# Kernel tuning notes

Measured on AMD Instinct MI355X. Metric: run time of the kernel, lower is better.

Reference implementation:

```python
import jax, jax.numpy as jnp
import numpy as np

D_MODEL = 1024
H = 16
D_K = D_MODEL // H


def setup_inputs() -> dict:
    key = jax.random.key(0)
    ks = jax.random.split(key, 12)
    B, S = 4, 2048
    s = 1.0 / np.sqrt(D_MODEL)
    return {
        "Q": jax.random.normal(ks[0], (B, S, D_MODEL), jnp.float32),
        "K": jax.random.normal(ks[1], (B, S, D_MODEL), jnp.float32),
        "V": jax.random.normal(ks[2], (B, S, D_MODEL), jnp.float32),
        "attn_mask": jnp.ones((B, S), jnp.int32),
        "Wq": jax.random.normal(ks[3], (D_MODEL, D_MODEL), jnp.float32) * s,
        "bq": jax.random.normal(ks[4], (D_MODEL,), jnp.float32) * s,
        "Wk": jax.random.normal(ks[5], (D_MODEL, D_MODEL), jnp.float32) * s,
        "bk": jax.random.normal(ks[6], (D_MODEL,), jnp.float32) * s,
        "Wv": jax.random.normal(ks[7], (D_MODEL, D_MODEL), jnp.float32) * s,
        "bv": jax.random.normal(ks[8], (D_MODEL,), jnp.float32) * s,
        "Wo": jax.random.normal(ks[9], (D_MODEL, D_MODEL), jnp.float32) * s,
        "bo": jax.random.normal(ks[10], (D_MODEL,), jnp.float32) * s,
    }


def _split_heads(x):
    B, S, _ = x.shape
    return x.reshape(B, S, H, D_K).transpose(0, 2, 1, 3)  # (B,H,S,Dk)


def reference(Q, K, V, attn_mask, Wq, bq, Wk, bk, Wv, bv, Wo, bo):
    # Linear projections (torch Linear: x @ W.T + b)
    q = _split_heads(Q @ Wq.T + bq)
    k = _split_heads(K @ Wk.T + bk)
    v = _split_heads(V @ Wv.T + bv)
    scale = 1.0 / jnp.sqrt(jnp.asarray(D_K, q.dtype))
    scores = jnp.einsum("bhqd,bhkd->bhqk", q, k) * scale  # (B,H,S,S)
    # 2-D mask (B,S) broadcast over heads and query positions; 0 -> -inf
    mask = attn_mask[:, None, None, :]
    scores = jnp.where(mask == 0, -jnp.inf, scores)
    attn = jax.nn.softmax(scores, axis=-1)
    # dropout_proba = 0.0 -> identity
    x = jnp.einsum("bhqk,bhkd->bhqd", attn, v)
    B, _, S, _ = x.shape
    x = x.transpose(0, 2, 1, 3).reshape(B, S, D_MODEL)
    return x @ Wo.T + bo
```

## Files before the change

kernel.cpp:

```cpp
#include <hip/hip_runtime.h>
#include <stdint.h>

typedef unsigned short u16;
typedef __attribute__((ext_vector_type(8))) unsigned short u16x8;
typedef __attribute__((ext_vector_type(4))) unsigned short u16x4;
typedef __attribute__((ext_vector_type(2))) __fp16 h16x2;
typedef __attribute__((ext_vector_type(4))) _Float16 f16x4;
typedef __attribute__((ext_vector_type(8))) _Float16 f16x8;
typedef __attribute__((ext_vector_type(4))) float f32x4;

#define MFMA16F16(a,b,c)  __builtin_amdgcn_mfma_f32_16x16x16f16((a),(b),(c),0,0,0)
#define MFMA32F16(a,b,c)  __builtin_amdgcn_mfma_f32_16x16x32_f16((a),(b),(c),0,0,0)

__device__ __forceinline__ f32x4 f4zero() {
    f32x4 z; z[0]=0.f; z[1]=0.f; z[2]=0.f; z[3]=0.f; return z;
}
__device__ __forceinline__ u16x8 cvth8(float4 a, float4 b) {
    union { h16x2 h[4]; u16x8 u; } U;
    U.h[0] = __builtin_amdgcn_cvt_pkrtz(a.x, a.y);
    U.h[1] = __builtin_amdgcn_cvt_pkrtz(a.z, a.w);
    U.h[2] = __builtin_amdgcn_cvt_pkrtz(b.x, b.y);
    U.h[3] = __builtin_amdgcn_cvt_pkrtz(b.z, b.w);
    return U.u;
}

#define GLDS(gp, lp) __builtin_amdgcn_global_load_lds( \
    (const __attribute__((address_space(1))) void*)(gp), \
    (__attribute__((address_space(3))) void*)(lp), 16, 0, 0)

#define QSC 0.1803368801111601f

__global__ __launch_bounds__(256) void conv_w(
    const float* __restrict__ w0, const float* __restrict__ w1,
    const float* __restrict__ w2, const float* __restrict__ w3,
    u16* __restrict__ out)
{
    const int t = blockIdx.x >> 8;
    const float* src = (t == 0) ? w0 : (t == 1) ? w1 : (t == 2) ? w2 : w3;
    const size_t idx = (size_t)(blockIdx.x & 255) * 4096 + (size_t)threadIdx.x * 16;
    u16* dst = out + (size_t)t * 1048576 + idx;
    float4 a0 = *(const float4*)(src + idx);
    float4 a1 = *(const float4*)(src + idx + 4);
    float4 a2 = *(const float4*)(src + idx + 8);
    float4 a3 = *(const float4*)(src + idx + 12);
    *(u16x8*)dst       = cvth8(a0, a1);
    *(u16x8*)(dst + 8) = cvth8(a2, a3);
}

template<int MODE>
__global__ __launch_bounds__(256, 3) void gemm_qkv(
    const float* __restrict__ Qf, const float* __restrict__ Kf, const float* __restrict__ Vf,
    const u16* __restrict__ wc,
    const float* __restrict__ Wqf, const float* __restrict__ Wkf, const float* __restrict__ Wvf,
    const float* __restrict__ bq, const float* __restrict__ bk, const float* __restrict__ bv,
    u16* __restrict__ qhp, u16* __restrict__ khp, u16* __restrict__ vtp)
{
    __shared__ __align__(16) u16 smem[24576];
    u16* Ct = smem;

    const int t  = blockIdx.y >> 3;
    const int n0 = (blockIdx.y & 7) * 128;
    const int m0 = blockIdx.x * 128;
    const float* X    = (t == 0) ? Qf : (t == 1) ? Kf : Vf;
    const float* Wf   = (t == 0) ? Wqf : (t == 1) ? Wkf : Wvf;
    const float* bias = (t == 0) ? bq : (t == 1) ? bk : bv;
    const u16*   Wb   = wc + (size_t)t * 1048576;
    u16*         dst  = (t == 0) ? qhp : (t == 1) ? khp : vtp;
    const float  scl  = (t == 0) ? QSC : 1.0f;

    const int tid  = threadIdx.x;
    const int wave = tid >> 6, lane = tid & 63;
    const int quad = lane >> 4, l16 = lane & 15;
    const int wm = (wave >> 1) * 64, wn = (wave & 1) * 64;

    const int srow = lane >> 2;
    const size_t scol = (size_t)(lane & 3) * 8;
    const int sr2 = tid >> 2, c2 = tid & 3;
    const float* Xb1 = X + (size_t)(m0 + sr2) * 1024 + c2 * 8;
    const float* Xb2 = Xb1 + (size_t)64 * 1024;
    const int sr = tid >> 1, hh = tid & 1;

    f32x4 acc[4][4];
    for (int i = 0; i < 4; i++) for (int j = 0; j < 4; j++) acc[i][j] = f4zero();

    auto stageB = [&](int b, int kt) {
        GLDS(Wb + (size_t)(n0 + wave * 32 +      srow) * 1024 + kt * 32 + scol,
             smem + b * 8192 + 4096 + wave * 1024);
        GLDS(Wb + (size_t)(n0 + wave * 32 + 16 + srow) * 1024 + kt * 32 + scol,
             smem + b * 8192 + 4096 + wave * 1024 + 512);
    };
    float4 xa_[4], xb_[4];
    auto loadXA = [&](int kt) {
        xa_[0] = *(const float4*)(Xb1 + kt * 32);     xa_[1] = *(const float4*)(Xb1 + kt * 32 + 4);
        xa_[2] = *(const float4*)(Xb2 + kt * 32);     xa_[3] = *(const float4*)(Xb2 + kt * 32 + 4);
    };
    auto loadXB = [&](int kt) {
        xb_[0] = *(const float4*)(Xb1 + kt * 32);     xb_[1] = *(const float4*)(Xb1 + kt * 32 + 4);
        xb_[2] = *(const float4*)(Xb2 + kt * 32);     xb_[3] = *(const float4*)(Xb2 + kt * 32 + 4);
    };
    auto writeXA = [&](int b) {
        u16* d = smem + b * 8192 + sr2 * 32 + c2 * 8;
        *(u16x8*)d          = cvth8(xa_[0], xa_[1]);
        *(u16x8*)(d + 2048) = cvth8(xa_[2], xa_[3]);
    };
    auto writeXB = [&](int b) {
        u16* d = smem + b * 8192 + sr2 * 32 + c2 * 8;
        *(u16x8*)d          = cvth8(xb_[0], xb_[1]);
        *(u16x8*)(d + 2048) = cvth8(xb_[2], xb_[3]);
    };
    auto comp = [&](int b) {
        const u16* As = smem + b * 8192;
        const u16* Bs = As + 4096;
        f16x8 af[4], bfr[4];
#pragma unroll
        for (int i = 0; i < 4; i++) {
            af[i]  = *(const f16x8*)(As + (wm + i * 16 + l16) * 32 + quad * 8);
            bfr[i] = *(const f16x8*)(Bs + (wn + i * 16 + l16) * 32 + quad * 8);
        }
        __builtin_amdgcn_s_setprio(1);
#pragma unroll
        for (int i = 0; i < 4; i++)
#pragma unroll
            for (int j = 0; j < 4; j++)
                acc[i][j] = MFMA32F16(af[i], bfr[j], acc[i][j]);
        __builtin_amdgcn_s_setprio(0);
    };

    if (MODE == 0) {
        for (int kt = 0; kt < 32; ++kt) {
            loadXA(kt); writeXA(0);
            const float* p = Wf + (size_t)(n0 + sr) * 1024 + kt * 32 + hh * 16;
            float4 b0 = *(const float4*)(p);     float4 b1 = *(const float4*)(p + 4);
            float4 b2 = *(const float4*)(p + 8); float4 b3 = *(const float4*)(p + 12);
            u16* d = smem + 4096 + sr * 32 + hh * 16;
            *(u16x8*)d       = cvth8(b0, b1);
            *(u16x8*)(d + 8) = cvth8(b2, b3);
            __syncthreads();
            comp(0);
            __syncthreads();
        }
    } else {
        stageB(0, 0);
        stageB(1, 1);
        loadXA(0); writeXA(0);
        loadXB(1);
        int bA = 0, bB = 1, bC = 2;
        for (int kt = 0; kt < 30; kt += 2) {
            asm volatile("s_waitcnt vmcnt(6) lgkmcnt(0)" ::: "memory");
            __builtin_amdgcn_s_barrier();
            __builtin_amdgcn_sched_barrier(0);
            loadXA(kt + 2);
            stageB(bC, kt + 2);
            comp(bA);
            __builtin_amdgcn_sched_barrier(0);
            writeXB(bB);
            { int tmp = bA; bA = bB; bB = bC; bC = tmp; }
            asm volatile("s_waitcnt vmcnt(6) lgkmcnt(0)" ::: "memory");
            __builtin_amdgcn_s_barrier();
            __builtin_amdgcn_sched_barrier(0);
            loadXB(kt + 3);
            stageB(bC, kt + 3);
            comp(bA);
            __builtin_amdgcn_sched_barrier(0);
            writeXA(bB);
            { int tmp = bA; bA = bB; bB = bC; bC = tmp; }
        }
        asm volatile("s_waitcnt vmcnt(6) lgkmcnt(0)" ::: "memory");
        __builtin_amdgcn_s_barrier();
        __builtin_amdgcn_sched_barrier(0);
        comp(bA);
        __builtin_amdgcn_sched_barrier(0);
        writeXB(bB);
        { int tmp = bA; bA = bB; bB = bC; bC = tmp; }
        asm volatile("s_waitcnt vmcnt(0) lgkmcnt(0)" ::: "memory");
        __builtin_amdgcn_s_barrier();
        __builtin_amdgcn_sched_barrier(0);
        comp(bA);
    }
    __syncthreads();

#pragma unroll
    for (int i = 0; i < 4; i++) {
        const int row = wm + i * 16 + quad * 4;
#pragma unroll
        for (int j = 0; j < 4; j++) {
            const int col = wn + j * 16 + l16;
            const float bv2 = bias[n0 + col];
#pragma unroll
            for (int r = 0; r < 2; r++) {
                union { h16x2 h; unsigned u; } P;
                P.h = __builtin_amdgcn_cvt_pkrtz((acc[i][j][2*r] + bv2) * scl,
                                                 (acc[i][j][2*r+1] + bv2) * scl);
                Ct[(row + 2*r)     * 136 + col] = (u16)(P.u & 0xFFFF);
                Ct[(row + 2*r + 1) * 136 + col] = (u16)(P.u >> 16);
            }
        }
    }
    __syncthreads();

    if (t < 2) {
        const int row = tid >> 1, half = tid & 1;
        const int m = m0 + row, b = m >> 11, s = m & 2047;
        const int h = (n0 >> 6) + half;
        u16* o = dst + ((size_t)(b * 16 + h) * 2048 + s) * 64;
        const u16* src = Ct + row * 136 + half * 64;
#pragma unroll
        for (int j = 0; j < 64; j += 8) *(u16x8*)(o + j) = *(const u16x8*)(src + j);
    } else {
        const int col = tid >> 1, shalf = tid & 1;
        const int h = (n0 >> 6) + (col >> 6), d = col & 63;
        const int mb = m0 + shalf * 64, b = mb >> 11, sb = mb & 2047;
        u16* o = dst + (size_t)((b * 16 + h) * 64 + d) * 2048 + sb;
#pragma unroll
        for (int j0 = 0; j0 < 64; j0 += 8) {
            u16x8 tv;
#pragma unroll
            for (int j = 0; j < 8; j++) tv[j] = Ct[(shalf * 64 + j0 + j) * 136 + col];
            *(u16x8*)(o + j0) = tv;
        }
    }
}

template<int MODE>
__global__ __launch_bounds__(256, 3) void gemm_o(
    const u16* __restrict__ Xb, const u16* __restrict__ wcO,
    const float* __restrict__ Wf, const float* __restrict__ bias,
    float* __restrict__ out)
{
    __shared__ __align__(16) u16 smem[24576];

    const int tid  = threadIdx.x;
    const int wave = tid >> 6, lane = tid & 63;
    const int quad = lane >> 4, l16 = lane & 15;
    const int m0 = blockIdx.x * 128, n0 = blockIdx.y * 128;
    const int wm = (wave >> 1) * 64, wn = (wave & 1) * 64;

    const int srow = lane >> 2;
    const size_t scol = (size_t)(lane & 3) * 8;
    const int sr = tid >> 1, hh = tid & 1;

    f32x4 acc[4][4];
    for (int i = 0; i < 4; i++) for (int j = 0; j < 4; j++) acc[i][j] = f4zero();

    auto stageA = [&](int b, int kt) {
        GLDS(Xb + (size_t)(m0 + wave * 32 +      srow) * 1024 + kt * 32 + scol,
             smem + b * 8192 + wave * 1024);
        GLDS(Xb + (size_t)(m0 + wave * 32 + 16 + srow) * 1024 + kt * 32 + scol,
             smem + b * 8192 + wave * 1024 + 512);
    };
    auto stageB = [&](int b, int kt) {
        GLDS(wcO + (size_t)(n0 + wave * 32 +      srow) * 1024 + kt * 32 + scol,
             smem + b * 8192 + 4096 + wave * 1024);
        GLDS(wcO + (size_t)(n0 + wave * 32 + 16 + srow) * 1024 + kt * 32 + scol,
             smem + b * 8192 + 4096 + wave * 1024 + 512);
    };
    float4 wr_[4];
    auto loadW = [&](int kt) {
        const float* p = Wf + (size_t)(n0 + sr) * 1024 + kt * 32 + hh * 16;
        wr_[0] = *(const float4*)(p);     wr_[1] = *(const float4*)(p + 4);
        wr_[2] = *(const float4*)(p + 8); wr_[3] = *(const float4*)(p + 12);
    };
    auto writeW = [&](int b) {
        u16* d = smem + b * 8192 + 4096 + sr * 32 + hh * 16;
        *(u16x8*)d       = cvth8(wr_[0], wr_[1]);
        *(u16x8*)(d + 8) = cvth8(wr_[2], wr_[3]);
    };
    auto comp = [&](int b) {
        const u16* As = smem + b * 8192;
        const u16* Bs = As + 4096;
        f16x8 af[4], bfr[4];
#pragma unroll
        for (int i = 0; i < 4; i++) {
            af[i]  = *(const f16x8*)(As + (wm + i * 16 + l16) * 32 + quad * 8);
            bfr[i] = *(const f16x8*)(Bs + (wn + i * 16 + l16) * 32 + quad * 8);
        }
        __builtin_amdgcn_s_setprio(1);
#pragma unroll
        for (int i = 0; i < 4; i++)
#pragma unroll
            for (int j = 0; j < 4; j++)
                acc[i][j] = MFMA32F16(af[i], bfr[j], acc[i][j]);
        __builtin_amdgcn_s_setprio(0);
    };

    stageA(0, 0);
    if (MODE == 2) stageB(0, 0);
    stageA(1, 1);
    if (MODE == 2) stageB(1, 1);
    if (MODE == 1) { loadW(0); writeW(0); }
    int bA = 0, bB = 1, bC = 2;
    for (int kt = 0; kt < 31; ++kt) {
        if (MODE == 2) asm volatile("s_waitcnt vmcnt(4) lgkmcnt(0)" ::: "memory");
        else           asm volatile("s_waitcnt vmcnt(2) lgkmcnt(0)" ::: "memory");
        __builtin_amdgcn_s_barrier();
        __builtin_amdgcn_sched_barrier(0);
        if (MODE == 1) loadW(kt + 1);
        if (kt < 30) {
            stageA(bC, kt + 2);
            if (MODE == 2) stageB(bC, kt + 2);
        }
        comp(bA);
        if (MODE == 1) writeW(bB);
        int tmp = bA; bA = bB; bB = bC; bC = tmp;
    }
    asm volatile("s_waitcnt vmcnt(0) lgkmcnt(0)" ::: "memory");
    __builtin_amdgcn_s_barrier();
    __builtin_amdgcn_sched_barrier(0);
    comp(bA);

#pragma unroll
    for (int i = 0; i < 4; i++)
#pragma unroll
        for (int j = 0; j < 4; j++) {
            const int col = wn + j * 16 + l16;
            const float bv = bias[n0 + col];
#pragma unroll
            for (int r = 0; r < 4; r++)
                out[(size_t)(m0 + wm + i * 16 + quad * 4 + r) * 1024 + n0 + col] = acc[i][j][r] + bv;
        }
}

__global__ __launch_bounds__(256, 4) void attn_fused(
    const u16* __restrict__ qh, const u16* __restrict__ kh,
    const u16* __restrict__ vth, const int* __restrict__ mask,
    u16* __restrict__ xout)
{
    __shared__ __align__(16) u16 Ksh[2][4096];
    __shared__ __align__(16) u16 Vsh[2][4352];
    __shared__ float mshf[2][64];

    const int tid = threadIdx.x, wave = tid >> 6, lane = tid & 63;
    const int quad = lane >> 4, l16 = lane & 15;

    const int flat = blockIdx.x + (blockIdx.y << 4);
    const int xr = flat & 7, xc_ = flat >> 3;
    const int qb = xc_ & 15, bh = xr + ((xc_ >> 4) << 3);
    const int b = bh >> 4, h = bh & 15;
    const int wq = qb * 128 + wave * 32;

    f16x8 qf[2][2];
#pragma unroll
    for (int qg = 0; qg < 2; qg++)
#pragma unroll
        for (int kc = 0; kc < 2; kc++)
            qf[qg][kc] = *(const f16x8*)(qh + ((size_t)bh * 2048 + wq + qg * 16 + l16) * 64
                                         + kc * 32 + quad * 8);

    f32x4 o[2][4];
#pragma unroll
    for (int qg = 0; qg < 2; qg++)
        for (int dt = 0; dt < 4; dt++) o[qg][dt] = f4zero();
    f32x4 lacc[2]; lacc[0] = f4zero(); lacc[1] = f4zero();
    f16x4 ones;
    ones[0] = (_Float16)1.f; ones[1] = (_Float16)1.f;
    ones[2] = (_Float16)1.f; ones[3] = (_Float16)1.f;

    const int klr = lane >> 3;
    const size_t kgoff = (size_t)((lane & 7) ^ klr) << 3;
    const u16* kgb = kh + (size_t)bh * 2048 * 64;

    const int skey = tid >> 2, sc = (tid & 3) * 16;
    const u16* vg = vth + ((size_t)bh * 64 + skey) * 2048 + sc;
    const int mrow = b * 2048;

    {
        GLDS(kgb + (size_t)(wave * 16 + klr) * 64 + kgoff,     &Ksh[0][wave * 1024]);
        GLDS(kgb + (size_t)(wave * 16 + 8 + klr) * 64 + kgoff, &Ksh[0][wave * 1024 + 512]);
        const u16x8 v0 = *(const u16x8*)(vg);
        const u16x8 v1 = *(const u16x8*)(vg + 8);
        u16* vd = &Vsh[0][skey * 68 + sc];
        *(u16x4*)(vd)      = (u16x4){v0[0], v0[1], v0[2], v0[3]};
        *(u16x4*)(vd + 4)  = (u16x4){v0[4], v0[5], v0[6], v0[7]};
        *(u16x4*)(vd + 8)  = (u16x4){v1[0], v1[1], v1[2], v1[3]};
        *(u16x4*)(vd + 12) = (u16x4){v1[4], v1[5], v1[6], v1[7]};
        if (tid < 64) mshf[0][tid] = mask[mrow + tid] ? -10.0f : -1.0e30f;
    }
    __syncthreads();

    for (int t = 0; t < 32; ++t) {
        const int cur = t & 1;
        const u16* Kc = &Ksh[cur][0];
        const u16* Vc = &Vsh[cur][0];

        u16x8 v0, v1; int mreg = 1;
        const int kk2 = (t + 1) * 64;
        if (t < 31) {
            GLDS(kgb + (size_t)(kk2 + wave * 16 + klr) * 64 + kgoff,
                 &Ksh[cur ^ 1][wave * 1024]);
            GLDS(kgb + (size_t)(kk2 + wave * 16 + 8 + klr) * 64 + kgoff,
                 &Ksh[cur ^ 1][wave * 1024 + 512]);
            v0 = *(const u16x8*)(vg + kk2);
            v1 = *(const u16x8*)(vg + kk2 + 8);
            if (tid < 64) mreg = mask[mrow + kk2 + tid];
        }

        __builtin_amdgcn_s_setprio(1);
        f16x4 pf[4][2];
#pragma unroll
        for (int nt = 0; nt < 4; nt++) {
            const int kro = (nt * 16 + l16) * 64;
            const f16x8 kf0 = *(const f16x8*)(Kc + kro + ((quad ^ (l16 & 7)) << 3));
            const f16x8 kf1 = *(const f16x8*)(Kc + kro + (((quad ^ 4) ^ (l16 & 7)) << 3));
            const float4 mb = *(const float4*)(&mshf[cur][nt * 16 + quad * 4]);
#pragma unroll
            for (int qg = 0; qg < 2; qg++) {
                f32x4 z;
                z[0] = mb.x; z[1] = mb.y; z[2] = mb.z; z[3] = mb.w;
                z = MFMA32F16(kf0, qf[qg][0], z);
                z = MFMA32F16(kf1, qf[qg][1], z);
                union { h16x2 h[2]; f16x4 v; } U;
                U.h[0] = __builtin_amdgcn_cvt_pkrtz(__builtin_amdgcn_exp2f(z[0]),
                                                    __builtin_amdgcn_exp2f(z[1]));
                U.h[1] = __builtin_amdgcn_cvt_pkrtz(__builtin_amdgcn_exp2f(z[2]),
                                                    __builtin_amdgcn_exp2f(z[3]));
                pf[nt][qg] = U.v;
            }
        }
#pragma unroll
        for (int nt = 0; nt < 4; nt++) {
            lacc[0] = MFMA16F16(ones, pf[nt][0], lacc[0]);
            lacc[1] = MFMA16F16(ones, pf[nt][1], lacc[1]);
        }
#pragma unroll
        for (int dt = 0; dt < 4; dt++) {
#pragma unroll
            for (int nt = 0; nt < 4; nt++) {
                const f16x4 vf = *(const f16x4*)(Vc + (dt * 16 + l16) * 68 + nt * 16 + quad * 4);
                o[0][dt] = MFMA16F16(vf, pf[nt][0], o[0][dt]);
                o[1][dt] = MFMA16F16(vf, pf[nt][1], o[1][dt]);
            }
        }
        __builtin_amdgcn_s_setprio(0);

        if (t < 31) {
            u16* vd = &Vsh[cur ^ 1][skey * 68 + sc];
            *(u16x4*)(vd)      = (u16x4){v0[0], v0[1], v0[2], v0[3]};
            *(u16x4*)(vd + 4)  = (u16x4){v0[4], v0[5], v0[6], v0[7]};
            *(u16x4*)(vd + 8)  = (u16x4){v1[0], v1[1], v1[2], v1[3]};
            *(u16x4*)(vd + 12) = (u16x4){v1[4], v1[5], v1[6], v1[7]};
            if (tid < 64) mshf[cur ^ 1][tid] = mreg ? -10.0f : -1.0e30f;
        }
        __syncthreads();
    }

#pragma unroll
    for (int qg = 0; qg < 2; qg++) {
        const float inv = 1.0f / lacc[qg][0];
        const int row = wq + qg * 16 + l16;
        u16* op = xout + ((size_t)b * 2048 + row) * 1024 + h * 64;
#pragma unroll
        for (int dt = 0; dt < 4; dt++) {
            union { h16x2 h[2]; u16x4 u; } U;
            U.h[0] = __builtin_amdgcn_cvt_pkrtz(o[qg][dt][0] * inv, o[qg][dt][1] * inv);
            U.h[1] = __builtin_amdgcn_cvt_pkrtz(o[qg][dt][2] * inv, o[qg][dt][3] * inv);
            *(u16x4*)(op + dt * 16 + quad * 4) = U.u;
        }
    }
}

extern "C" void kernel_launch(void* const* d_in, const int* in_sizes, int n_in,
                              void* d_out, int out_size, void* d_ws, size_t ws_size,
                              hipStream_t stream)
{
    const float* Q   = (const float*)d_in[0];
    const float* K   = (const float*)d_in[1];
    const float* V   = (const float*)d_in[2];
    const int*   msk = (const int*)d_in[3];
    const float* Wq  = (const float*)d_in[4];
    const float* bq  = (const float*)d_in[5];
    const float* Wk  = (const float*)d_in[6];
    const float* bk  = (const float*)d_in[7];
    const float* Wv  = (const float*)d_in[8];
    const float* bv  = (const float*)d_in[9];
    const float* Wo  = (const float*)d_in[10];
    const float* bo  = (const float*)d_in[11];

    u16* base = (u16*)d_ws;
    dim3 blk(256);
    dim3 gq(64, 24);
    dim3 ga(16, 64);
    dim3 go(64, 8);

    if (ws_size >= ((size_t)72 << 20)) {
        u16* wc  = base;
        u16* qhp = base + 4194304;
        u16* khp = qhp + 8388608;
        u16* vtp = khp + 8388608;
        u16* xs  = vtp + 8388608;
        conv_w<<<1024, blk, 0, stream>>>(Wq, Wk, Wv, Wo, wc);
        gemm_qkv<1><<<gq, blk, 0, stream>>>(Q, K, V, wc,
            nullptr, nullptr, nullptr, bq, bk, bv, qhp, khp, vtp);
        attn_fused<<<ga, blk, 0, stream>>>(qhp, khp, vtp, msk, xs);
        gemm_o<2><<<go, blk, 0, stream>>>(xs, wc + 3 * 1048576, nullptr, bo, (float*)d_out);
    } else {
        u16* qhp = base;
        u16* khp = qhp + 8388608;
        u16* vtp = khp + 8388608;
        u16* xs  = vtp + 8388608;
        gemm_qkv<0><<<gq, blk, 0, stream>>>(Q, K, V, nullptr,
            Wq, Wk, Wv, bq, bk, bv, qhp, khp, vtp);
        attn_fused<<<ga, blk, 0, stream>>>(qhp, khp, vtp, msk, xs);
        gemm_o<1><<<go, blk, 0, stream>>>(xs, nullptr, Wo, bo, (float*)d_out);
    }
}
```

Measured before the change: 345.9 us.

## Shrink GEMM smem to double buffers and narrow output-projection tiles for occupancy

The QKV projection GEMM moves from a triple-buffered LDS pipeline to a double-buffered one with explicit waits and barriers. This cuts shared memory so the launch bound can rise to four blocks per CU. The output-projection GEMM uses 128x64 tiles with a simple double-buffered pipeline and less LDS, and its grid doubles to 64x16. The trade is more barriers and less prefetch depth in exchange for higher occupancy and more blocks.

```diff
diff --git a/kernel.cpp b/kernel.cpp
--- a/kernel.cpp
+++ b/kernel.cpp
@@ -48,14 +48,14 @@
 }
 
 template<int MODE>
-__global__ __launch_bounds__(256, 3) void gemm_qkv(
+__global__ __launch_bounds__(256, 4) void gemm_qkv(
     const float* __restrict__ Qf, const float* __restrict__ Kf, const float* __restrict__ Vf,
     const u16* __restrict__ wc,
     const float* __restrict__ Wqf, const float* __restrict__ Wkf, const float* __restrict__ Wvf,
     const float* __restrict__ bq, const float* __restrict__ bk, const float* __restrict__ bv,
     u16* __restrict__ qhp, u16* __restrict__ khp, u16* __restrict__ vtp)
 {
-    __shared__ __align__(16) u16 smem[24576];
+    __shared__ __align__(16) u16 smem[17408];
     u16* Ct = smem;
 
     const int t  = blockIdx.y >> 3;
@@ -140,42 +140,47 @@
             __syncthreads();
         }
     } else {
+        loadXA(0); writeXA(0);
         stageB(0, 0);
-        stageB(1, 1);
-        loadXA(0); writeXA(0);
         loadXB(1);
-        int bA = 0, bB = 1, bC = 2;
+        asm volatile("s_waitcnt lgkmcnt(0)" ::: "memory");
+        __builtin_amdgcn_s_barrier();
+        __builtin_amdgcn_sched_barrier(0);
         for (int kt = 0; kt < 30; kt += 2) {
-            asm volatile("s_waitcnt vmcnt(6) lgkmcnt(0)" ::: "memory");
+            loadXA(kt + 2);
+            stageB(1, kt + 1);
+            asm volatile("s_waitcnt vmcnt(6)" ::: "memory");
             __builtin_amdgcn_s_barrier();
             __builtin_amdgcn_sched_barrier(0);
-            loadXA(kt + 2);
-            stageB(bC, kt + 2);
-            comp(bA);
-            __builtin_amdgcn_sched_barrier(0);
-            writeXB(bB);
-            { int tmp = bA; bA = bB; bB = bC; bC = tmp; }
-            asm volatile("s_waitcnt vmcnt(6) lgkmcnt(0)" ::: "memory");
+            comp(0);
+            writeXB(1);
+            asm volatile("s_waitcnt lgkmcnt(0)" ::: "memory");
             __builtin_amdgcn_s_barrier();
             __builtin_amdgcn_sched_barrier(0);
             loadXB(kt + 3);
-            stageB(bC, kt + 3);
-            comp(bA);
+            stageB(0, kt + 2);
+            asm volatile("s_waitcnt vmcnt(6)" ::: "memory");
+            __builtin_amdgcn_s_barrier();
             __builtin_amdgcn_sched_barrier(0);
-            writeXA(bB);
-            { int tmp = bA; bA = bB; bB = bC; bC = tmp; }
-        }
-        asm volatile("s_waitcnt vmcnt(6) lgkmcnt(0)" ::: "memory");
+            comp(1);
+            writeXA(0);
+            asm volatile("s_waitcnt lgkmcnt(0)" ::: "memory");
+            __builtin_amdgcn_s_barrier();
+            __builtin_amdgcn_sched_barrier(0);
+        }
+        stageB(1, 31);
+        asm volatile("s_waitcnt vmcnt(2)" ::: "memory");
         __builtin_amdgcn_s_barrier();
         __builtin_amdgcn_sched_barrier(0);
-        comp(bA);
-        __builtin_amdgcn_sched_barrier(0);
-        writeXB(bB);
-        { int tmp = bA; bA = bB; bB = bC; bC = tmp; }
-        asm volatile("s_waitcnt vmcnt(0) lgkmcnt(0)" ::: "memory");
+        comp(0);
+        writeXB(1);
+        asm volatile("s_waitcnt lgkmcnt(0)" ::: "memory");
         __builtin_amdgcn_s_barrier();
         __builtin_amdgcn_sched_barrier(0);
-        comp(bA);
+        asm volatile("s_waitcnt vmcnt(0)" ::: "memory");
+        __builtin_amdgcn_s_barrier();
+        __builtin_amdgcn_sched_barrier(0);
+        comp(1);
     }
     __syncthreads();
 
@@ -222,96 +227,85 @@
 }
 
 template<int MODE>
-__global__ __launch_bounds__(256, 3) void gemm_o(
+__global__ __launch_bounds__(256, 4) void gemm_o(
     const u16* __restrict__ Xb, const u16* __restrict__ wcO,
     const float* __restrict__ Wf, const float* __restrict__ bias,
     float* __restrict__ out)
 {
-    __shared__ __align__(16) u16 smem[24576];
+    __shared__ __align__(16) u16 smem[12288];
 
     const int tid  = threadIdx.x;
     const int wave = tid >> 6, lane = tid & 63;
     const int quad = lane >> 4, l16 = lane & 15;
-    const int m0 = blockIdx.x * 128, n0 = blockIdx.y * 128;
-    const int wm = (wave >> 1) * 64, wn = (wave & 1) * 64;
+    const int m0 = blockIdx.x * 128, n0 = blockIdx.y * 64;
+    const int wm = (wave >> 1) * 64, wn = (wave & 1) * 32;
 
     const int srow = lane >> 2;
     const size_t scol = (size_t)(lane & 3) * 8;
-    const int sr = tid >> 1, hh = tid & 1;
-
-    f32x4 acc[4][4];
-    for (int i = 0; i < 4; i++) for (int j = 0; j < 4; j++) acc[i][j] = f4zero();
-
-    auto stageA = [&](int b, int kt) {
+    const int sr = tid >> 2, hc = tid & 3;
+
+    f32x4 acc[4][2];
+    for (int i = 0; i < 4; i++) for (int j = 0; j < 2; j++) acc[i][j] = f4zero();
+
+    auto stageAB = [&](int b, int kt) {
         GLDS(Xb + (size_t)(m0 + wave * 32 +      srow) * 1024 + kt * 32 + scol,
-             smem + b * 8192 + wave * 1024);
+             smem + b * 6144 + wave * 1024);
         GLDS(Xb + (size_t)(m0 + wave * 32 + 16 + srow) * 1024 + kt * 32 + scol,
-             smem + b * 8192 + wave * 1024 + 512);
-    };
-    auto stageB = [&](int b, int kt) {
-        GLDS(wcO + (size_t)(n0 + wave * 32 +      srow) * 1024 + kt * 32 + scol,
-             smem + b * 8192 + 4096 + wave * 1024);
-        GLDS(wcO + (size_t)(n0 + wave * 32 + 16 + srow) * 1024 + kt * 32 + scol,
-             smem + b * 8192 + 4096 + wave * 1024 + 512);
-    };
-    float4 wr_[4];
-    auto loadW = [&](int kt) {
-        const float* p = Wf + (size_t)(n0 + sr) * 1024 + kt * 32 + hh * 16;
-        wr_[0] = *(const float4*)(p);     wr_[1] = *(const float4*)(p + 4);
-        wr_[2] = *(const float4*)(p + 8); wr_[3] = *(const float4*)(p + 12);
-    };
-    auto writeW = [&](int b) {
-        u16* d = smem + b * 8192 + 4096 + sr * 32 + hh * 16;
-        *(u16x8*)d       = cvth8(wr_[0], wr_[1]);
-        *(u16x8*)(d + 8) = cvth8(wr_[2], wr_[3]);
+             smem + b * 6144 + wave * 1024 + 512);
+        if (MODE == 2)
+            GLDS(wcO + (size_t)(n0 + wave * 16 + srow) * 1024 + kt * 32 + scol,
+                 smem + b * 6144 + 4096 + wave * 512);
     };
     auto comp = [&](int b) {
-        const u16* As = smem + b * 8192;
+        const u16* As = smem + b * 6144;
         const u16* Bs = As + 4096;
-        f16x8 af[4], bfr[4];
-#pragma unroll
-        for (int i = 0; i < 4; i++) {
+        f16x8 af[4], bfr[2];
+#pragma unroll
+        for (int i = 0; i < 4; i++)
             af[i]  = *(const f16x8*)(As + (wm + i * 16 + l16) * 32 + quad * 8);
-            bfr[i] = *(const f16x8*)(Bs + (wn + i * 16 + l16) * 32 + quad * 8);
-        }
+#pragma unroll
+        for (int j = 0; j < 2; j++)
+            bfr[j] = *(const f16x8*)(Bs + (wn + j * 16 + l16) * 32 + quad * 8);
         __builtin_amdgcn_s_setprio(1);
 #pragma unroll
         for (int i = 0; i < 4; i++)
 #pragma unroll
-            for (int j = 0; j < 4; j++)
+            for (int j = 0; j < 2; j++)
                 acc[i][j] = MFMA32F16(af[i], bfr[j], acc[i][j]);
         __builtin_amdgcn_s_setprio(0);
     };
 
-    stageA(0, 0);
-    if (MODE == 2) stageB(0, 0);
-    stageA(1, 1);
-    if (MODE == 2) stageB(1, 1);
-    if (MODE == 1) { loadW(0); writeW(0); }
-    int bA = 0, bB = 1, bC = 2;
-    for (int kt = 0; kt < 31; ++kt) {
-        if (MODE == 2) asm volatile("s_waitcnt vmcnt(4) lgkmcnt(0)" ::: "memory");
-        else           asm volatile("s_waitcnt vmcnt(2) lgkmcnt(0)" ::: "memory");
+    if (MODE == 1) {
+        for (int kt = 0; kt < 32; ++kt) {
+            stageAB(0, kt);
+            const float* p = Wf + (size_t)(n0 + sr) * 1024 + kt * 32 + hc * 8;
+            float4 b0 = *(const float4*)(p);
+            float4 b1 = *(const float4*)(p + 4);
+            *(u16x8*)(smem + 4096 + sr * 32 + hc * 8) = cvth8(b0, b1);
+            __syncthreads();
+            comp(0);
+            __syncthreads();
+        }
+    } else {
+        stageAB(0, 0);
+        for (int kt = 0; kt < 31; ++kt) {
+            stageAB((kt + 1) & 1, kt + 1);
+            asm volatile("s_waitcnt vmcnt(3)" ::: "memory");
+            __builtin_amdgcn_s_barrier();
+            __builtin_amdgcn_sched_barrier(0);
+            comp(kt & 1);
+            __builtin_amdgcn_s_barrier();
+        }
+        asm volatile("s_waitcnt vmcnt(0)" ::: "memory");
         __builtin_amdgcn_s_barrier();
         __builtin_amdgcn_sched_barrier(0);
-        if (MODE == 1) loadW(kt + 1);
-        if (kt < 30) {
-            stageA(bC, kt + 2);
-            if (MODE == 2) stageB(bC, kt + 2);
-        }
-        comp(bA);
-        if (MODE == 1) writeW(bB);
-        int tmp = bA; bA = bB; bB = bC; bC = tmp;
-    }
-    asm volatile("s_waitcnt vmcnt(0) lgkmcnt(0)" ::: "memory");
-    __builtin_amdgcn_s_barrier();
-    __builtin_amdgcn_sched_barrier(0);
-    comp(bA);
+        comp(1);
+    }
 
 #pragma unroll
     for (int i = 0; i < 4; i++)
 #pragma unroll
-        for (int j = 0; j < 4; j++) {
+        for (int j = 0; j < 2; j++) {
             const int col = wn + j * 16 + l16;
             const float bv = bias[n0 + col];
 #pragma unroll
@@ -479,7 +473,7 @@
     dim3 blk(256);
     dim3 gq(64, 24);
     dim3 ga(16, 64);
-    dim3 go(64, 8);
+    dim3 go(64, 16);
 
     if (ws_size >= ((size_t)72 << 20)) {
         u16* wc  = base;
```

Result: slower. 479.7 us (+38.7%).

## Widen QKV GEMM K-tile to 64 with swizzled LDS and grouped block order

Applied to the files above, without the earlier changes.

Restructures the QKV projection GEMM main loop to use 64-wide K tiles with double buffering instead of 32-wide triple buffering. LDS rows gain an XOR swizzle to avoid bank conflicts, and blocks are remapped to group M-tiles for better L2 reuse. This halves the number of barriers per K step, at the cost of more LDS per block and a lower occupancy target (launch bounds 3 to 2 blocks).

```diff
diff --git a/kernel.cpp b/kernel.cpp
--- a/kernel.cpp
+++ b/kernel.cpp
@@ -48,19 +48,22 @@
 }
 
 template<int MODE>
-__global__ __launch_bounds__(256, 3) void gemm_qkv(
+__global__ __launch_bounds__(256, 2) void gemm_qkv(
     const float* __restrict__ Qf, const float* __restrict__ Kf, const float* __restrict__ Vf,
     const u16* __restrict__ wc,
     const float* __restrict__ Wqf, const float* __restrict__ Wkf, const float* __restrict__ Wvf,
     const float* __restrict__ bq, const float* __restrict__ bk, const float* __restrict__ bv,
     u16* __restrict__ qhp, u16* __restrict__ khp, u16* __restrict__ vtp)
 {
-    __shared__ __align__(16) u16 smem[24576];
+    __shared__ __align__(16) u16 smem[32768];
     u16* Ct = smem;
 
-    const int t  = blockIdx.y >> 3;
-    const int n0 = (blockIdx.y & 7) * 128;
-    const int m0 = blockIdx.x * 128;
+    const int flat = blockIdx.x + (int)blockIdx.y * 64;
+    const int g    = ((flat >> 6) << 3) | (flat & 7);
+    const int t    = g >> 6;
+    const int m0   = (g & 63) * 128;
+    const int n0   = ((flat >> 3) & 7) * 128;
+
     const float* X    = (t == 0) ? Qf : (t == 1) ? Kf : Vf;
     const float* Wf   = (t == 0) ? Wqf : (t == 1) ? Wkf : Wvf;
     const float* bias = (t == 0) ? bq : (t == 1) ? bk : bv;
@@ -73,109 +76,132 @@
     const int quad = lane >> 4, l16 = lane & 15;
     const int wm = (wave >> 1) * 64, wn = (wave & 1) * 64;
 
-    const int srow = lane >> 2;
-    const size_t scol = (size_t)(lane & 3) * 8;
-    const int sr2 = tid >> 2, c2 = tid & 3;
-    const float* Xb1 = X + (size_t)(m0 + sr2) * 1024 + c2 * 8;
-    const float* Xb2 = Xb1 + (size_t)64 * 1024;
+    const int glr = lane >> 3;
+    const size_t gsw = (size_t)(((lane & 7) ^ glr) << 3);
+    const int xrw = tid >> 1, xh = tid & 1;
+    const float* Xb = X + (size_t)(m0 + xrw) * 1024 + xh * 32;
     const int sr = tid >> 1, hh = tid & 1;
 
     f32x4 acc[4][4];
     for (int i = 0; i < 4; i++) for (int j = 0; j < 4; j++) acc[i][j] = f4zero();
 
     auto stageB = [&](int b, int kt) {
-        GLDS(Wb + (size_t)(n0 + wave * 32 +      srow) * 1024 + kt * 32 + scol,
-             smem + b * 8192 + 4096 + wave * 1024);
-        GLDS(Wb + (size_t)(n0 + wave * 32 + 16 + srow) * 1024 + kt * 32 + scol,
-             smem + b * 8192 + 4096 + wave * 1024 + 512);
-    };
-    float4 xa_[4], xb_[4];
+        u16* base = smem + b * 16384 + 8192 + wave * 2048;
+#pragma unroll
+        for (int r = 0; r < 4; r++)
+            GLDS(Wb + (size_t)(n0 + wave * 32 + r * 8 + glr) * 1024 + kt * 64 + gsw,
+                 base + r * 512);
+    };
+    float4 xa_[8], xb_[8];
     auto loadXA = [&](int kt) {
-        xa_[0] = *(const float4*)(Xb1 + kt * 32);     xa_[1] = *(const float4*)(Xb1 + kt * 32 + 4);
-        xa_[2] = *(const float4*)(Xb2 + kt * 32);     xa_[3] = *(const float4*)(Xb2 + kt * 32 + 4);
+#pragma unroll
+        for (int j = 0; j < 8; j++) xa_[j] = *(const float4*)(Xb + kt * 64 + j * 4);
     };
     auto loadXB = [&](int kt) {
-        xb_[0] = *(const float4*)(Xb1 + kt * 32);     xb_[1] = *(const float4*)(Xb1 + kt * 32 + 4);
-        xb_[2] = *(const float4*)(Xb2 + kt * 32);     xb_[3] = *(const float4*)(Xb2 + kt * 32 + 4);
+#pragma unroll
+        for (int j = 0; j < 8; j++) xb_[j] = *(const float4*)(Xb + kt * 64 + j * 4);
     };
     auto writeXA = [&](int b) {
-        u16* d = smem + b * 8192 + sr2 * 32 + c2 * 8;
-        *(u16x8*)d          = cvth8(xa_[0], xa_[1]);
-        *(u16x8*)(d + 2048) = cvth8(xa_[2], xa_[3]);
+        u16* base = smem + b * 16384 + xrw * 64;
+#pragma unroll
+        for (int cc = 0; cc < 4; cc++) {
+            const int c = xh * 4 + cc;
+            *(u16x8*)(base + ((c ^ (xrw & 7)) << 3)) = cvth8(xa_[2*cc], xa_[2*cc+1]);
+        }
     };
     auto writeXB = [&](int b) {
-        u16* d = smem + b * 8192 + sr2 * 32 + c2 * 8;
-        *(u16x8*)d          = cvth8(xb_[0], xb_[1]);
-        *(u16x8*)(d + 2048) = cvth8(xb_[2], xb_[3]);
+        u16* base = smem + b * 16384 + xrw * 64;
+#pragma unroll
+        for (int cc = 0; cc < 4; cc++) {
+            const int c = xh * 4 + cc;
+            *(u16x8*)(base + ((c ^ (xrw & 7)) << 3)) = cvth8(xb_[2*cc], xb_[2*cc+1]);
+        }
     };
     auto comp = [&](int b) {
-        const u16* As = smem + b * 8192;
-        const u16* Bs = As + 4096;
-        f16x8 af[4], bfr[4];
-#pragma unroll
-        for (int i = 0; i < 4; i++) {
-            af[i]  = *(const f16x8*)(As + (wm + i * 16 + l16) * 32 + quad * 8);
-            bfr[i] = *(const f16x8*)(Bs + (wn + i * 16 + l16) * 32 + quad * 8);
-        }
-        __builtin_amdgcn_s_setprio(1);
-#pragma unroll
-        for (int i = 0; i < 4; i++)
-#pragma unroll
-            for (int j = 0; j < 4; j++)
-                acc[i][j] = MFMA32F16(af[i], bfr[j], acc[i][j]);
-        __builtin_amdgcn_s_setprio(0);
+        const u16* As = smem + b * 16384;
+        const u16* Bs = As + 8192;
+#pragma unroll
+        for (int kk = 0; kk < 2; kk++) {
+            f16x8 af[4], bfr[4];
+#pragma unroll
+            for (int i = 0; i < 4; i++) {
+                const int ra = wm + i * 16 + l16, rb = wn + i * 16 + l16;
+                af[i]  = *(const f16x8*)(As + ra * 64 + (((kk * 4 + quad) ^ (ra & 7)) << 3));
+                bfr[i] = *(const f16x8*)(Bs + rb * 64 + (((kk * 4 + quad) ^ (rb & 7)) << 3));
+            }
+            __builtin_amdgcn_s_setprio(1);
+#pragma unroll
+            for (int i = 0; i < 4; i++)
+#pragma unroll
+                for (int j = 0; j < 4; j++)
+                    acc[i][j] = MFMA32F16(af[i], bfr[j], acc[i][j]);
+            __builtin_amdgcn_s_setprio(0);
+        }
     };
 
     if (MODE == 0) {
+        u16* As = smem;
+        u16* Bs = smem + 4096;
         for (int kt = 0; kt < 32; ++kt) {
-            loadXA(kt); writeXA(0);
+            const float* px = X + (size_t)(m0 + sr) * 1024 + kt * 32 + hh * 16;
+            float4 a0 = *(const float4*)(px);     float4 a1 = *(const float4*)(px + 4);
+            float4 a2 = *(const float4*)(px + 8); float4 a3 = *(const float4*)(px + 12);
+            u16* da = As + sr * 32 + hh * 16;
+            *(u16x8*)da       = cvth8(a0, a1);
+            *(u16x8*)(da + 8) = cvth8(a2, a3);
             const float* p = Wf + (size_t)(n0 + sr) * 1024 + kt * 32 + hh * 16;
             float4 b0 = *(const float4*)(p);     float4 b1 = *(const float4*)(p + 4);
             float4 b2 = *(const float4*)(p + 8); float4 b3 = *(const float4*)(p + 12);
-            u16* d = smem + 4096 + sr * 32 + hh * 16;
+            u16* d = Bs + sr * 32 + hh * 16;
             *(u16x8*)d       = cvth8(b0, b1);
             *(u16x8*)(d + 8) = cvth8(b2, b3);
             __syncthreads();
-            comp(0);
+            f16x8 af[4], bfr[4];
+#pragma unroll
+            for (int i = 0; i < 4; i++) {
+                af[i]  = *(const f16x8*)(As + (wm + i * 16 + l16) * 32 + quad * 8);
+                bfr[i] = *(const f16x8*)(Bs + (wn + i * 16 + l16) * 32 + quad * 8);
+            }
+#pragma unroll
+            for (int i = 0; i < 4; i++)
+#pragma unroll
+                for (int j = 0; j < 4; j++)
+                    acc[i][j] = MFMA32F16(af[i], bfr[j], acc[i][j]);
             __syncthreads();
         }
     } else {
         stageB(0, 0);
-        stageB(1, 1);
         loadXA(0); writeXA(0);
         loadXB(1);
-        int bA = 0, bB = 1, bC = 2;
-        for (int kt = 0; kt < 30; kt += 2) {
-            asm volatile("s_waitcnt vmcnt(6) lgkmcnt(0)" ::: "memory");
+        for (int kt = 0; kt < 14; kt += 2) {
+            asm volatile("s_waitcnt vmcnt(8) lgkmcnt(0)" ::: "memory");
             __builtin_amdgcn_s_barrier();
             __builtin_amdgcn_sched_barrier(0);
+            stageB((kt + 1) & 1, kt + 1);
             loadXA(kt + 2);
-            stageB(bC, kt + 2);
-            comp(bA);
+            comp(kt & 1);
             __builtin_amdgcn_sched_barrier(0);
-            writeXB(bB);
-            { int tmp = bA; bA = bB; bB = bC; bC = tmp; }
-            asm volatile("s_waitcnt vmcnt(6) lgkmcnt(0)" ::: "memory");
+            writeXB((kt + 1) & 1);
+            asm volatile("s_waitcnt vmcnt(8) lgkmcnt(0)" ::: "memory");
             __builtin_amdgcn_s_barrier();
             __builtin_amdgcn_sched_barrier(0);
+            stageB((kt + 2) & 1, kt + 2);
             loadXB(kt + 3);
-            stageB(bC, kt + 3);
-            comp(bA);
+            comp((kt + 1) & 1);
             __builtin_amdgcn_sched_barrier(0);
-            writeXA(bB);
-            { int tmp = bA; bA = bB; bB = bC; bC = tmp; }
-        }
-        asm volatile("s_waitcnt vmcnt(6) lgkmcnt(0)" ::: "memory");
+            writeXA((kt + 2) & 1);
+        }
+        asm volatile("s_waitcnt vmcnt(8) lgkmcnt(0)" ::: "memory");
         __builtin_amdgcn_s_barrier();
         __builtin_amdgcn_sched_barrier(0);
-        comp(bA);
+        stageB(1, 15);
+        comp(0);
         __builtin_amdgcn_sched_barrier(0);
-        writeXB(bB);
-        { int tmp = bA; bA = bB; bB = bC; bC = tmp; }
+        writeXB(1);
         asm volatile("s_waitcnt vmcnt(0) lgkmcnt(0)" ::: "memory");
         __builtin_amdgcn_s_barrier();
         __builtin_amdgcn_sched_barrier(0);
-        comp(bA);
+        comp(1);
     }
     __syncthreads();
 
```

Result: slower. 383.5 us (+10.9%).
